# Optimization experiments

Hardware: AMD Instinct MI355X
Metric: run time of the kernel (lower is better)

The kernel has to match this reference:

```python
import jax, jax.numpy as jnp
import numpy as np

N_NODES = 100000

def gcn_conv(x, W, b, src, dst, n):
    # PyG GCNConv with add_self_loops=True, symmetric normalization.
    # Transform first (reduces feature dim before irregular aggregation).
    h = x @ W  # [N, out]
    # degree with self loops: in-degree over dst plus 1 per node
    deg = jax.ops.segment_sum(jnp.ones_like(dst, dtype=h.dtype), dst, num_segments=n) + 1.0
    dinv = jax.lax.rsqrt(deg)  # deg >= 1 due to self loops
    norm = dinv[src] * dinv[dst]  # [E]
    # message = norm * h[src], aggregated at dst; self-loop term = dinv_i^2 * h_i
    agg = jax.ops.segment_sum(h[src] * norm[:, None], dst, num_segments=n)
    agg = agg + h * (dinv * dinv)[:, None]
    return agg + b

def setup_inputs() -> dict:
    key = jax.random.key(0)
    k1, k2, k3, k4, k5 = jax.random.split(key, 5)
    F_in, H, E_dim = 128, 64, 64
    node_features = jax.random.normal(k1, (N_NODES, F_in), dtype=jnp.float32)
    edge_index = jax.random.randint(k2, (2, 1600000), 0, N_NODES, dtype=jnp.int64)
    s = 1.0 / np.sqrt(F_in)
    W1 = jax.random.uniform(k3, (F_in, H), jnp.float32, -s, s)
    b1 = jnp.zeros((H,), jnp.float32)
    s2 = 1.0 / np.sqrt(H)
    W2 = jax.random.uniform(k4, (H, H), jnp.float32, -s2, s2)
    b2 = jnp.zeros((H,), jnp.float32)
    Wl = jax.random.uniform(k5, (H, E_dim), jnp.float32, -s2, s2)
    bl = jnp.zeros((E_dim,), jnp.float32)
    return {"node_features": node_features, "edge_index": edge_index,
            "W1": W1, "b1": b1, "W2": W2, "b2": b2, "Wl": Wl, "bl": bl}

def reference(node_features, edge_index, W1, b1, W2, b2, Wl, bl):
    src, dst = edge_index[0], edge_index[1]
    n = node_features.shape[0]
    x = node_features.astype(jnp.float32)
    x = jax.nn.relu(gcn_conv(x, W1, b1, src, dst, n))
    # dropout: train=False -> identity
    x = jax.nn.relu(gcn_conv(x, W2, b2, src, dst, n))
    x = x @ Wl + bl
    return jax.nn.sigmoid(x).T  # [embed_size, N]
```

## Files before the change

kernel.cpp:

```cpp
#include <hip/hip_runtime.h>
#include <hip/hip_bf16.h>


#define FEAT 64
#define FIN 128
#define PAD 64
#define SUBC 4
#define SUBCAP 1280
#define CAP (SUBC * SUBCAP)
#define EPB 8192
#define MAXNB 512

typedef __attribute__((ext_vector_type(8))) short  short8;
typedef __attribute__((ext_vector_type(4))) float  f32x4;
typedef __attribute__((ext_vector_type(2))) float  float2v;

__device__ __forceinline__ unsigned short f2bf(float f) {
    union { float f; unsigned u; } x; x.f = f;
    unsigned r = x.u + 0x7FFF + ((x.u >> 16) & 1);
    return (unsigned short)(r >> 16);
}
__device__ __forceinline__ float bflo(unsigned u) {
    union { unsigned v; float f; } x; x.v = u << 16; return x.f;
}
__device__ __forceinline__ float bfhi(unsigned u) {
    union { unsigned v; float f; } x; x.v = u & 0xFFFF0000u; return x.f;
}

__global__ void wtrans_kernel(const float* __restrict__ W1, const float* __restrict__ W2,
                              const float* __restrict__ Wl,
                              unsigned short* __restrict__ Wt1, unsigned short* __restrict__ Wt2,
                              unsigned short* __restrict__ Wlt, int* __restrict__ bcnt) {
    int t = blockIdx.x * 256 + threadIdx.x;
    if (t < FIN * 64) {
        int k = t >> 6, n = t & 63;
        Wt1[n * FIN + k] = f2bf(W1[t]);
    } else if (t < FIN * 64 + 64 * 64) {
        int u = t - FIN * 64;
        int k = u >> 6, n = u & 63;
        Wt2[n * 64 + k] = f2bf(W2[u]);
    } else if (t < FIN * 64 + 2 * 64 * 64) {
        int u = t - FIN * 64 - 64 * 64;
        int k = u >> 6, n = u & 63;
        Wlt[n * 64 + k] = f2bf(Wl[u]);
    } else if (t < FIN * 64 + 2 * 64 * 64 + MAXNB * SUBC * 16) {
        bcnt[t - FIN * 64 - 2 * 64 * 64] = 0;
    }
}

__global__ __launch_bounds__(256) void bin_kernel(const int* __restrict__ ei,
                                                  int* __restrict__ bcnt,
                                                  int* __restrict__ bbuf,
                                                  int E, int nb) {
    __shared__ int hist[MAXNB];
    __shared__ int base[MAXNB];
    for (int t = threadIdx.x; t < nb; t += 256) hist[t] = 0;
    __syncthreads();
    int e0 = blockIdx.x * EPB;
    int sub = blockIdx.x & (SUBC - 1);
    int sreg[32], dreg[32], preg[32];
#pragma unroll
    for (int k = 0; k < 32; ++k) {
        int idx = e0 + k * 256 + threadIdx.x;
        if (idx < E) {
            sreg[k] = ei[idx];
            dreg[k] = ei[E + idx];
            preg[k] = atomicAdd(&hist[dreg[k] >> 8], 1);
        } else {
            dreg[k] = -1;
        }
    }
    __syncthreads();
    for (int t = threadIdx.x; t < nb; t += 256) {
        int h = hist[t];
        base[t] = (h > 0) ? atomicAdd(&bcnt[(t * SUBC + sub) * 16], h) : 0;
    }
    __syncthreads();
#pragma unroll
    for (int k = 0; k < 32; ++k) {
        if (dreg[k] >= 0) {
            int b = dreg[k] >> 8;
            int p = base[b] + preg[k];
            if (p < SUBCAP)
                bbuf[(size_t)b * CAP + sub * SUBCAP + p] = sreg[k] | ((dreg[k] & 255) << 20);
        }
    }
}

__global__ __launch_bounds__(256) void ell_from_bins_kernel(const int* __restrict__ bbuf,
                                                            const int* __restrict__ bcnt,
                                                            int* __restrict__ col,
                                                            int* __restrict__ cnt,
                                                            float* __restrict__ dinv,
                                                            unsigned int* __restrict__ gz,
                                                            int N) {
    __shared__ int lcnt[256];
    int b = blockIdx.x;
    int d0 = b << 8;
    lcnt[threadIdx.x] = 0;
    if (b == 0 && threadIdx.x < 32)
        gz[(size_t)N * 32 + threadIdx.x] = 0u;
    __syncthreads();
#pragma unroll
    for (int sub = 0; sub < SUBC; ++sub) {
        int ne = bcnt[(b * SUBC + sub) * 16];
        if (ne > SUBCAP) ne = SUBCAP;
        const int* eb = bbuf + (size_t)b * CAP + sub * SUBCAP;
        for (int i = threadIdx.x; i < ne; i += 256) {
            int w = eb[i];
            int s = w & 0xFFFFF;
            int dl = w >> 20;
            int slot = atomicAdd(&lcnt[dl], 1);
            if (slot < PAD) col[(size_t)(d0 + dl) * PAD + slot] = s;
        }
    }
    __syncthreads();
    int d = d0 + threadIdx.x;
    if (d < N) {
        int c = lcnt[threadIdx.x];
        if (c > PAD) c = PAD;
        int c8 = (c + 7) & ~7;
        for (int k = c; k < c8; ++k) col[(size_t)d * PAD + k] = N;
        cnt[d] = c;
        dinv[d] = rsqrtf((float)c + 1.0f);
    }
}

__global__ __launch_bounds__(256) void gemm1_mfma_kernel(const float* __restrict__ x,
                                                         const unsigned short* __restrict__ Wt,
                                                         const float* __restrict__ dinv,
                                                         unsigned short* __restrict__ g, int N) {
    const int lane = threadIdx.x & 63;
    const int wave = threadIdx.x >> 6;
    const int m = lane & 15, quad = lane >> 4;
    const int r0 = blockIdx.x * 64 + wave * 16;
    const int arow = r0 + m;
    const bool aok = arow < N;
    f32x4 acc[4] = {f32x4{0,0,0,0}, f32x4{0,0,0,0}, f32x4{0,0,0,0}, f32x4{0,0,0,0}};
    union { short8 s; unsigned short u[8]; } a;
#pragma unroll
    for (int s = 0; s < FIN / 32; ++s) {
        if (aok) {
            const float* xp = x + (size_t)arow * FIN + s * 32 + quad * 8;
            float4 a0 = *(const float4*)xp;
            float4 a1 = *(const float4*)(xp + 4);
            a.u[0] = f2bf(a0.x); a.u[1] = f2bf(a0.y);
            a.u[2] = f2bf(a0.z); a.u[3] = f2bf(a0.w);
            a.u[4] = f2bf(a1.x); a.u[5] = f2bf(a1.y);
            a.u[6] = f2bf(a1.z); a.u[7] = f2bf(a1.w);
        } else {
#pragma unroll
            for (int k = 0; k < 8; ++k) a.u[k] = 0;
        }
#pragma unroll
        for (int t = 0; t < 4; ++t) {
            const unsigned short* bp = Wt + (size_t)(t * 16 + m) * FIN + s * 32 + quad * 8;
            short8 bf = *(const short8*)bp;
            acc[t] = __builtin_amdgcn_mfma_f32_16x16x32_bf16(a.s, bf, acc[t], 0, 0, 0);
        }
    }
    const int rbase = r0 + quad * 4;
#pragma unroll
    for (int i = 0; i < 4; ++i) {
        int r = rbase + i;
        if (r < N) {
            float di = dinv[r];
#pragma unroll
            for (int t = 0; t < 4; ++t)
                g[(size_t)r * 64 + t * 16 + m] = f2bf(di * acc[t][i]);
        }
    }
}

__global__ __launch_bounds__(256) void gemm2_mfma_kernel(const unsigned short* __restrict__ xb,
                                                         const unsigned short* __restrict__ Wt,
                                                         const float* __restrict__ dinv,
                                                         unsigned short* __restrict__ g, int N) {
    const int lane = threadIdx.x & 63;
    const int wave = threadIdx.x >> 6;
    const int m = lane & 15, quad = lane >> 4;
    const int r0 = blockIdx.x * 64 + wave * 16;
    const int arow = r0 + m;
    const bool aok = arow < N;
    f32x4 acc[4] = {f32x4{0,0,0,0}, f32x4{0,0,0,0}, f32x4{0,0,0,0}, f32x4{0,0,0,0}};
    const short8 zero8 = short8{0,0,0,0,0,0,0,0};
#pragma unroll
    for (int s = 0; s < 2; ++s) {
        short8 a = aok ? *(const short8*)(xb + (size_t)arow * 64 + s * 32 + quad * 8) : zero8;
#pragma unroll
        for (int t = 0; t < 4; ++t) {
            short8 bf = *(const short8*)(Wt + (size_t)(t * 16 + m) * 64 + s * 32 + quad * 8);
            acc[t] = __builtin_amdgcn_mfma_f32_16x16x32_bf16(a, bf, acc[t], 0, 0, 0);
        }
    }
    const int rbase = r0 + quad * 4;
#pragma unroll
    for (int i = 0; i < 4; ++i) {
        int r = rbase + i;
        if (r < N) {
            float di = dinv[r];
#pragma unroll
            for (int t = 0; t < 4; ++t)
                g[(size_t)r * 64 + t * 16 + m] = f2bf(di * acc[t][i]);
        }
    }
}

__global__ __launch_bounds__(256) void agg_relu_kernel(const unsigned short* __restrict__ g,
                                                       const int* __restrict__ cnt,
                                                       const int* __restrict__ col,
                                                       const float* __restrict__ dinv,
                                                       const float* __restrict__ b,
                                                       unsigned short* __restrict__ xout, int N) {
    const int lane = threadIdx.x & 63;
    const int wave = threadIdx.x >> 6;
    const int ng = lane >> 3, fc = lane & 7;
    const int node = blockIdx.x * 32 + wave * 8 + ng;
    const bool valid = node < N;
    int c8 = 0;
    if (valid) {
        int c = cnt[node];
        if (c > PAD) c = PAD;
        c8 = (c + 7) & ~7;
    }
    int cmax = c8;
#pragma unroll
    for (int mk = 8; mk <= 32; mk <<= 1) {
        int o = __shfl_xor(cmax, mk, 64);
        cmax = cmax > o ? cmax : o;
    }
    const int* cl = col + (size_t)node * PAD;
    float2v acc0 = {0.f, 0.f}, acc1 = {0.f, 0.f}, acc2 = {0.f, 0.f}, acc3 = {0.f, 0.f};
    {
        uint4 w = *(const uint4*)(g + (size_t)(valid ? node : N) * 64 + fc * 8);
        acc0 += (float2v){bflo(w.x), bfhi(w.x)};
        acc1 += (float2v){bflo(w.y), bfhi(w.y)};
        acc2 += (float2v){bflo(w.z), bfhi(w.z)};
        acc3 += (float2v){bflo(w.w), bfhi(w.w)};
    }
    for (int j = 0; j < cmax; j += 4) {
        bool ok = j < c8;
        int s0 = ok ? cl[j]     : N;
        int s1 = ok ? cl[j + 1] : N;
        int s2 = ok ? cl[j + 2] : N;
        int s3 = ok ? cl[j + 3] : N;
        uint4 w0 = *(const uint4*)(g + (size_t)s0 * 64 + fc * 8);
        uint4 w1 = *(const uint4*)(g + (size_t)s1 * 64 + fc * 8);
        uint4 w2 = *(const uint4*)(g + (size_t)s2 * 64 + fc * 8);
        uint4 w3 = *(const uint4*)(g + (size_t)s3 * 64 + fc * 8);
        acc0 += (float2v){bflo(w0.x), bfhi(w0.x)};
        acc1 += (float2v){bflo(w0.y), bfhi(w0.y)};
        acc2 += (float2v){bflo(w0.z), bfhi(w0.z)};
        acc3 += (float2v){bflo(w0.w), bfhi(w0.w)};
        acc0 += (float2v){bflo(w1.x), bfhi(w1.x)};
        acc1 += (float2v){bflo(w1.y), bfhi(w1.y)};
        acc2 += (float2v){bflo(w1.z), bfhi(w1.z)};
        acc3 += (float2v){bflo(w1.w), bfhi(w1.w)};
        acc0 += (float2v){bflo(w2.x), bfhi(w2.x)};
        acc1 += (float2v){bflo(w2.y), bfhi(w2.y)};
        acc2 += (float2v){bflo(w2.z), bfhi(w2.z)};
        acc3 += (float2v){bflo(w2.w), bfhi(w2.w)};
        acc0 += (float2v){bflo(w3.x), bfhi(w3.x)};
        acc1 += (float2v){bflo(w3.y), bfhi(w3.y)};
        acc2 += (float2v){bflo(w3.z), bfhi(w3.z)};
        acc3 += (float2v){bflo(w3.w), bfhi(w3.w)};
    }
    if (valid) {
        float di = dinv[node];
        float4 b0 = *(const float4*)&b[fc * 8];
        float4 b1 = *(const float4*)&b[fc * 8 + 4];
        union { uint4 v; unsigned short u[8]; } o;
        o.u[0] = f2bf(fmaxf(di * acc0.x + b0.x, 0.f));
        o.u[1] = f2bf(fmaxf(di * acc0.y + b0.y, 0.f));
        o.u[2] = f2bf(fmaxf(di * acc1.x + b0.z, 0.f));
        o.u[3] = f2bf(fmaxf(di * acc1.y + b0.w, 0.f));
        o.u[4] = f2bf(fmaxf(di * acc2.x + b1.x, 0.f));
        o.u[5] = f2bf(fmaxf(di * acc2.y + b1.y, 0.f));
        o.u[6] = f2bf(fmaxf(di * acc3.x + b1.z, 0.f));
        o.u[7] = f2bf(fmaxf(di * acc3.y + b1.w, 0.f));
        *(uint4*)&xout[(size_t)node * 64 + fc * 8] = o.v;
    }
}

__global__ __launch_bounds__(256) void final_mfma_kernel(const unsigned short* __restrict__ x2,
                                                         const unsigned short* __restrict__ Wlt,
                                                         const float* __restrict__ bl,
                                                         float* __restrict__ out, int N) {
    const int lane = threadIdx.x & 63;
    const int wave = threadIdx.x >> 6;
    const int m = lane & 15, quad = lane >> 4;
    const int r0 = blockIdx.x * 64 + wave * 16;
    const int arow = r0 + m;
    const bool aok = arow < N;
    f32x4 acc[4] = {f32x4{0,0,0,0}, f32x4{0,0,0,0}, f32x4{0,0,0,0}, f32x4{0,0,0,0}};
    const short8 zero8 = short8{0,0,0,0,0,0,0,0};
#pragma unroll
    for (int s = 0; s < 2; ++s) {
        short8 a = aok ? *(const short8*)(x2 + (size_t)arow * 64 + s * 32 + quad * 8) : zero8;
#pragma unroll
        for (int t = 0; t < 4; ++t) {
            short8 bf = *(const short8*)(Wlt + (size_t)(t * 16 + m) * 64 + s * 32 + quad * 8);
            acc[t] = __builtin_amdgcn_mfma_f32_16x16x32_bf16(a, bf, acc[t], 0, 0, 0);
        }
    }
    const int rbase = r0 + quad * 4;
    if (rbase + 3 < N && (N & 3) == 0) {
#pragma unroll
        for (int t = 0; t < 4; ++t) {
            int j = t * 16 + m;
            float bj = bl[j];
            float4 o;
            o.x = 1.f / (1.f + __expf(-(acc[t][0] + bj)));
            o.y = 1.f / (1.f + __expf(-(acc[t][1] + bj)));
            o.z = 1.f / (1.f + __expf(-(acc[t][2] + bj)));
            o.w = 1.f / (1.f + __expf(-(acc[t][3] + bj)));
            *(float4*)&out[(size_t)j * N + rbase] = o;
        }
    } else {
#pragma unroll
        for (int t = 0; t < 4; ++t) {
            int j = t * 16 + m;
            float bj = bl[j];
#pragma unroll
            for (int i = 0; i < 4; ++i) {
                int r = rbase + i;
                if (r < N)
                    out[(size_t)j * N + r] = 1.f / (1.f + __expf(-(acc[t][i] + bj)));
            }
        }
    }
}

extern "C" void kernel_launch(void* const* d_in, const int* in_sizes, int n_in,
                              void* d_out, int out_size, void* d_ws, size_t ws_size,
                              hipStream_t stream) {
    const float* x   = (const float*)d_in[0];
    const int*   ei  = (const int*)d_in[1];
    const float* W1  = (const float*)d_in[2];
    const float* b1  = (const float*)d_in[3];
    const float* W2  = (const float*)d_in[4];
    const float* b2  = (const float*)d_in[5];
    const float* Wl  = (const float*)d_in[6];
    const float* bl  = (const float*)d_in[7];
    float*       out = (float*)d_out;

    int N  = in_sizes[0] / FIN;
    int E  = in_sizes[1] / 2;
    int nb = (N + 255) >> 8;
    int ng = (N + 63) >> 6;

    int*            bcnt = (int*)d_ws;
    unsigned short* Wt1  = (unsigned short*)(bcnt + MAXNB * SUBC * 16);
    unsigned short* Wt2  = Wt1 + FIN * 64;
    unsigned short* Wlt  = Wt2 + 64 * 64;
    int*            cnt  = (int*)(Wlt + 64 * 64);
    float*          dinv = (float*)(cnt + N);
    int*            col  = (int*)(dinv + N);
    int*            bbuf = col + (size_t)N * PAD;
    unsigned short* bufG = (unsigned short*)bbuf;
    unsigned short* bufX = bufG + (size_t)(N + 1) * FEAT;

    int wtot = FIN * 64 + 2 * 64 * 64 + MAXNB * SUBC * 16;
    wtrans_kernel<<<(wtot + 255) / 256, 256, 0, stream>>>(W1, W2, Wl, Wt1, Wt2, Wlt, bcnt);

    bin_kernel<<<(E + EPB - 1) / EPB, 256, 0, stream>>>(ei, bcnt, bbuf, E, nb);
    ell_from_bins_kernel<<<nb, 256, 0, stream>>>(bbuf, bcnt, col, cnt, dinv,
                                                 (unsigned int*)bufG, N);

    gemm1_mfma_kernel<<<ng, 256, 0, stream>>>(x, Wt1, dinv, bufG, N);
    agg_relu_kernel<<<(N + 31) / 32, 256, 0, stream>>>(bufG, cnt, col, dinv, b1, bufX, N);

    gemm2_mfma_kernel<<<ng, 256, 0, stream>>>(bufX, Wt2, dinv, bufG, N);
    agg_relu_kernel<<<(N + 31) / 32, 256, 0, stream>>>(bufG, cnt, col, dinv, b2, bufX, N);

    final_mfma_kernel<<<ng, 256, 0, stream>>>(bufX, Wlt, bl, out, N);
}
```

Measured before the change: 251.5 us.

## Fuse aggregation with following GEMMs via shared-memory tile

Merges each aggregation+ReLU pass with the next dense transform (W2 or the final linear+sigmoid) in one 512-thread block. The aggregated 64-node tile is staged in LDS and fed to MFMA, so the intermediate activations no longer round-trip through global memory and two launches go away. The dinv array is dropped and rsqrt is recomputed from cnt wherever it is needed. The gather loop now loads column indices with int4 vector loads and handles 8 neighbours per iteration. The block-wide barrier and extra LDS may reduce occupancy. The per-node ELL count is no longer clamped to PAD before use, which only matters if a node has more than PAD in-edges.

```diff
diff --git a/kernel.cpp b/kernel.cpp
--- a/kernel.cpp
+++ b/kernel.cpp
@@ -91,15 +91,17 @@
                                                             const int* __restrict__ bcnt,
                                                             int* __restrict__ col,
                                                             int* __restrict__ cnt,
-                                                            float* __restrict__ dinv,
                                                             unsigned int* __restrict__ gz,
+                                                            unsigned int* __restrict__ gz2,
                                                             int N) {
     __shared__ int lcnt[256];
     int b = blockIdx.x;
     int d0 = b << 8;
     lcnt[threadIdx.x] = 0;
-    if (b == 0 && threadIdx.x < 32)
+    if (b == 0 && threadIdx.x < 32) {
         gz[(size_t)N * 32 + threadIdx.x] = 0u;
+        gz2[(size_t)N * 32 + threadIdx.x] = 0u;
+    }
     __syncthreads();
 #pragma unroll
     for (int sub = 0; sub < SUBC; ++sub) {
@@ -122,13 +124,12 @@
         int c8 = (c + 7) & ~7;
         for (int k = c; k < c8; ++k) col[(size_t)d * PAD + k] = N;
         cnt[d] = c;
-        dinv[d] = rsqrtf((float)c + 1.0f);
     }
 }
 
 __global__ __launch_bounds__(256) void gemm1_mfma_kernel(const float* __restrict__ x,
                                                          const unsigned short* __restrict__ Wt,
-                                                         const float* __restrict__ dinv,
+                                                         const int* __restrict__ cnt,
                                                          unsigned short* __restrict__ g, int N) {
     const int lane = threadIdx.x & 63;
     const int wave = threadIdx.x >> 6;
@@ -164,7 +165,7 @@
     for (int i = 0; i < 4; ++i) {
         int r = rbase + i;
         if (r < N) {
-            float di = dinv[r];
+            float di = rsqrtf((float)cnt[r] + 1.0f);
 #pragma unroll
             for (int t = 0; t < 4; ++t)
                 g[(size_t)r * 64 + t * 16 + m] = f2bf(di * acc[t][i]);
@@ -172,142 +173,161 @@
     }
 }
 
-__global__ __launch_bounds__(256) void gemm2_mfma_kernel(const unsigned short* __restrict__ xb,
-                                                         const unsigned short* __restrict__ Wt,
-                                                         const float* __restrict__ dinv,
-                                                         unsigned short* __restrict__ g, int N) {
-    const int lane = threadIdx.x & 63;
-    const int wave = threadIdx.x >> 6;
+
+#define AGG_PHASE(bvec)                                                          \
+    const int lane = threadIdx.x & 63;                                           \
+    const int wave = threadIdx.x >> 6;                                           \
+    const int ngi = lane >> 3, fc = lane & 7;                                    \
+    const int nloc = wave * 8 + ngi;                                             \
+    const int node = blockIdx.x * 64 + nloc;                                     \
+    const bool valid = node < N;                                                 \
+    int c8 = 0;                                                                  \
+    float di = 0.f;                                                              \
+    if (valid) {                                                                 \
+        int c = cnt[node];                                                       \
+        di = rsqrtf((float)c + 1.0f);                                            \
+        c8 = (c + 7) & ~7;                                                       \
+    }                                                                            \
+    int cmax = c8;                                                               \
+    _Pragma("unroll")                                                            \
+    for (int mk = 8; mk <= 32; mk <<= 1) {                                       \
+        int o = __shfl_xor(cmax, mk, 64);                                        \
+        cmax = cmax > o ? cmax : o;                                              \
+    }                                                                            \
+    const int* cl = col + (size_t)node * PAD;                                    \
+    float2v acc0 = {0.f, 0.f}, acc1 = {0.f, 0.f}, acc2 = {0.f, 0.f}, acc3 = {0.f, 0.f}; \
+    {                                                                            \
+        uint4 w = *(const uint4*)(g + (size_t)(valid ? node : N) * 64 + fc * 8); \
+        acc0 += (float2v){bflo(w.x), bfhi(w.x)};                                 \
+        acc1 += (float2v){bflo(w.y), bfhi(w.y)};                                 \
+        acc2 += (float2v){bflo(w.z), bfhi(w.z)};                                 \
+        acc3 += (float2v){bflo(w.w), bfhi(w.w)};                                 \
+    }                                                                            \
+    const int4 sent = {N, N, N, N};                                              \
+    for (int j = 0; j < cmax; j += 8) {                                          \
+        bool ok = j < c8;                                                        \
+        int4 ca = ok ? *(const int4*)(cl + j)     : sent;                        \
+        int4 cb = ok ? *(const int4*)(cl + j + 4) : sent;                        \
+        uint4 w0 = *(const uint4*)(g + (size_t)ca.x * 64 + fc * 8);              \
+        uint4 w1 = *(const uint4*)(g + (size_t)ca.y * 64 + fc * 8);              \
+        uint4 w2 = *(const uint4*)(g + (size_t)ca.z * 64 + fc * 8);              \
+        uint4 w3 = *(const uint4*)(g + (size_t)ca.w * 64 + fc * 8);              \
+        uint4 w4 = *(const uint4*)(g + (size_t)cb.x * 64 + fc * 8);              \
+        uint4 w5 = *(const uint4*)(g + (size_t)cb.y * 64 + fc * 8);              \
+        uint4 w6 = *(const uint4*)(g + (size_t)cb.z * 64 + fc * 8);              \
+        uint4 w7 = *(const uint4*)(g + (size_t)cb.w * 64 + fc * 8);              \
+        acc0 += (float2v){bflo(w0.x), bfhi(w0.x)};                               \
+        acc1 += (float2v){bflo(w0.y), bfhi(w0.y)};                               \
+        acc2 += (float2v){bflo(w0.z), bfhi(w0.z)};                               \
+        acc3 += (float2v){bflo(w0.w), bfhi(w0.w)};                               \
+        acc0 += (float2v){bflo(w1.x), bfhi(w1.x)};                               \
+        acc1 += (float2v){bflo(w1.y), bfhi(w1.y)};                               \
+        acc2 += (float2v){bflo(w1.z), bfhi(w1.z)};                               \
+        acc3 += (float2v){bflo(w1.w), bfhi(w1.w)};                               \
+        acc0 += (float2v){bflo(w2.x), bfhi(w2.x)};                               \
+        acc1 += (float2v){bflo(w2.y), bfhi(w2.y)};                               \
+        acc2 += (float2v){bflo(w2.z), bfhi(w2.z)};                               \
+        acc3 += (float2v){bflo(w2.w), bfhi(w2.w)};                               \
+        acc0 += (float2v){bflo(w3.x), bfhi(w3.x)};                               \
+        acc1 += (float2v){bflo(w3.y), bfhi(w3.y)};                               \
+        acc2 += (float2v){bflo(w3.z), bfhi(w3.z)};                               \
+        acc3 += (float2v){bflo(w3.w), bfhi(w3.w)};                               \
+        acc0 += (float2v){bflo(w4.x), bfhi(w4.x)};                               \
+        acc1 += (float2v){bflo(w4.y), bfhi(w4.y)};                               \
+        acc2 += (float2v){bflo(w4.z), bfhi(w4.z)};                               \
+        acc3 += (float2v){bflo(w4.w), bfhi(w4.w)};                               \
+        acc0 += (float2v){bflo(w5.x), bfhi(w5.x)};                               \
+        acc1 += (float2v){bflo(w5.y), bfhi(w5.y)};                               \
+        acc2 += (float2v){bflo(w5.z), bfhi(w5.z)};                               \
+        acc3 += (float2v){bflo(w5.w), bfhi(w5.w)};                               \
+        acc0 += (float2v){bflo(w6.x), bfhi(w6.x)};                               \
+        acc1 += (float2v){bflo(w6.y), bfhi(w6.y)};                               \
+        acc2 += (float2v){bflo(w6.z), bfhi(w6.z)};                               \
+        acc3 += (float2v){bflo(w6.w), bfhi(w6.w)};                               \
+        acc0 += (float2v){bflo(w7.x), bfhi(w7.x)};                               \
+        acc1 += (float2v){bflo(w7.y), bfhi(w7.y)};                               \
+        acc2 += (float2v){bflo(w7.z), bfhi(w7.z)};                               \
+        acc3 += (float2v){bflo(w7.w), bfhi(w7.w)};                               \
+    }                                                                            \
+    {                                                                            \
+        float4 b0 = *(const float4*)&bvec[fc * 8];                               \
+        float4 b1 = *(const float4*)&bvec[fc * 8 + 4];                           \
+        union { uint4 v; unsigned short u[8]; } o;                               \
+        o.u[0] = f2bf(fmaxf(di * acc0.x + b0.x, 0.f));                           \
+        o.u[1] = f2bf(fmaxf(di * acc0.y + b0.y, 0.f));                           \
+        o.u[2] = f2bf(fmaxf(di * acc1.x + b0.z, 0.f));                           \
+        o.u[3] = f2bf(fmaxf(di * acc1.y + b0.w, 0.f));                           \
+        o.u[4] = f2bf(fmaxf(di * acc2.x + b1.x, 0.f));                           \
+        o.u[5] = f2bf(fmaxf(di * acc2.y + b1.y, 0.f));                           \
+        o.u[6] = f2bf(fmaxf(di * acc3.x + b1.z, 0.f));                           \
+        o.u[7] = f2bf(fmaxf(di * acc3.y + b1.w, 0.f));                           \
+        *(uint4*)&tile[nloc][fc * 8] = o.v;                                      \
+    }                                                                            \
+    __syncthreads();
+
+__global__ __launch_bounds__(512) void agg_gemm2_kernel(const unsigned short* __restrict__ g,
+                                                        const int* __restrict__ cnt,
+                                                        const int* __restrict__ col,
+                                                        const float* __restrict__ b,
+                                                        const unsigned short* __restrict__ Wt,
+                                                        unsigned short* __restrict__ gout,
+                                                        int N) {
+    __shared__ unsigned short tile[64][72];
+    AGG_PHASE(b)
+    const int v = wave & 3;
+    const int tb = (wave >> 2) * 2;
     const int m = lane & 15, quad = lane >> 4;
-    const int r0 = blockIdx.x * 64 + wave * 16;
-    const int arow = r0 + m;
-    const bool aok = arow < N;
-    f32x4 acc[4] = {f32x4{0,0,0,0}, f32x4{0,0,0,0}, f32x4{0,0,0,0}, f32x4{0,0,0,0}};
-    const short8 zero8 = short8{0,0,0,0,0,0,0,0};
+    f32x4 acc[2] = {f32x4{0,0,0,0}, f32x4{0,0,0,0}};
 #pragma unroll
     for (int s = 0; s < 2; ++s) {
-        short8 a = aok ? *(const short8*)(xb + (size_t)arow * 64 + s * 32 + quad * 8) : zero8;
-#pragma unroll
-        for (int t = 0; t < 4; ++t) {
-            short8 bf = *(const short8*)(Wt + (size_t)(t * 16 + m) * 64 + s * 32 + quad * 8);
+        short8 a = *(const short8*)&tile[v * 16 + m][s * 32 + quad * 8];
+#pragma unroll
+        for (int t = 0; t < 2; ++t) {
+            short8 bf = *(const short8*)(Wt + (size_t)((tb + t) * 16 + m) * 64 + s * 32 + quad * 8);
             acc[t] = __builtin_amdgcn_mfma_f32_16x16x32_bf16(a, bf, acc[t], 0, 0, 0);
         }
     }
-    const int rbase = r0 + quad * 4;
+    const int rbase = blockIdx.x * 64 + v * 16 + quad * 4;
 #pragma unroll
     for (int i = 0; i < 4; ++i) {
         int r = rbase + i;
         if (r < N) {
-            float di = dinv[r];
-#pragma unroll
-            for (int t = 0; t < 4; ++t)
-                g[(size_t)r * 64 + t * 16 + m] = f2bf(di * acc[t][i]);
-        }
-    }
-}
-
-__global__ __launch_bounds__(256) void agg_relu_kernel(const unsigned short* __restrict__ g,
-                                                       const int* __restrict__ cnt,
-                                                       const int* __restrict__ col,
-                                                       const float* __restrict__ dinv,
-                                                       const float* __restrict__ b,
-                                                       unsigned short* __restrict__ xout, int N) {
-    const int lane = threadIdx.x & 63;
-    const int wave = threadIdx.x >> 6;
-    const int ng = lane >> 3, fc = lane & 7;
-    const int node = blockIdx.x * 32 + wave * 8 + ng;
-    const bool valid = node < N;
-    int c8 = 0;
-    if (valid) {
-        int c = cnt[node];
-        if (c > PAD) c = PAD;
-        c8 = (c + 7) & ~7;
-    }
-    int cmax = c8;
-#pragma unroll
-    for (int mk = 8; mk <= 32; mk <<= 1) {
-        int o = __shfl_xor(cmax, mk, 64);
-        cmax = cmax > o ? cmax : o;
-    }
-    const int* cl = col + (size_t)node * PAD;
-    float2v acc0 = {0.f, 0.f}, acc1 = {0.f, 0.f}, acc2 = {0.f, 0.f}, acc3 = {0.f, 0.f};
-    {
-        uint4 w = *(const uint4*)(g + (size_t)(valid ? node : N) * 64 + fc * 8);
-        acc0 += (float2v){bflo(w.x), bfhi(w.x)};
-        acc1 += (float2v){bflo(w.y), bfhi(w.y)};
-        acc2 += (float2v){bflo(w.z), bfhi(w.z)};
-        acc3 += (float2v){bflo(w.w), bfhi(w.w)};
-    }
-    for (int j = 0; j < cmax; j += 4) {
-        bool ok = j < c8;
-        int s0 = ok ? cl[j]     : N;
-        int s1 = ok ? cl[j + 1] : N;
-        int s2 = ok ? cl[j + 2] : N;
-        int s3 = ok ? cl[j + 3] : N;
-        uint4 w0 = *(const uint4*)(g + (size_t)s0 * 64 + fc * 8);
-        uint4 w1 = *(const uint4*)(g + (size_t)s1 * 64 + fc * 8);
-        uint4 w2 = *(const uint4*)(g + (size_t)s2 * 64 + fc * 8);
-        uint4 w3 = *(const uint4*)(g + (size_t)s3 * 64 + fc * 8);
-        acc0 += (float2v){bflo(w0.x), bfhi(w0.x)};
-        acc1 += (float2v){bflo(w0.y), bfhi(w0.y)};
-        acc2 += (float2v){bflo(w0.z), bfhi(w0.z)};
-        acc3 += (float2v){bflo(w0.w), bfhi(w0.w)};
-        acc0 += (float2v){bflo(w1.x), bfhi(w1.x)};
-        acc1 += (float2v){bflo(w1.y), bfhi(w1.y)};
-        acc2 += (float2v){bflo(w1.z), bfhi(w1.z)};
-        acc3 += (float2v){bflo(w1.w), bfhi(w1.w)};
-        acc0 += (float2v){bflo(w2.x), bfhi(w2.x)};
-        acc1 += (float2v){bflo(w2.y), bfhi(w2.y)};
-        acc2 += (float2v){bflo(w2.z), bfhi(w2.z)};
-        acc3 += (float2v){bflo(w2.w), bfhi(w2.w)};
-        acc0 += (float2v){bflo(w3.x), bfhi(w3.x)};
-        acc1 += (float2v){bflo(w3.y), bfhi(w3.y)};
-        acc2 += (float2v){bflo(w3.z), bfhi(w3.z)};
-        acc3 += (float2v){bflo(w3.w), bfhi(w3.w)};
-    }
-    if (valid) {
-        float di = dinv[node];
-        float4 b0 = *(const float4*)&b[fc * 8];
-        float4 b1 = *(const float4*)&b[fc * 8 + 4];
-        union { uint4 v; unsigned short u[8]; } o;
-        o.u[0] = f2bf(fmaxf(di * acc0.x + b0.x, 0.f));
-        o.u[1] = f2bf(fmaxf(di * acc0.y + b0.y, 0.f));
-        o.u[2] = f2bf(fmaxf(di * acc1.x + b0.z, 0.f));
-        o.u[3] = f2bf(fmaxf(di * acc1.y + b0.w, 0.f));
-        o.u[4] = f2bf(fmaxf(di * acc2.x + b1.x, 0.f));
-        o.u[5] = f2bf(fmaxf(di * acc2.y + b1.y, 0.f));
-        o.u[6] = f2bf(fmaxf(di * acc3.x + b1.z, 0.f));
-        o.u[7] = f2bf(fmaxf(di * acc3.y + b1.w, 0.f));
-        *(uint4*)&xout[(size_t)node * 64 + fc * 8] = o.v;
-    }
-}
-
-__global__ __launch_bounds__(256) void final_mfma_kernel(const unsigned short* __restrict__ x2,
-                                                         const unsigned short* __restrict__ Wlt,
-                                                         const float* __restrict__ bl,
-                                                         float* __restrict__ out, int N) {
-    const int lane = threadIdx.x & 63;
-    const int wave = threadIdx.x >> 6;
+            float dr = rsqrtf((float)cnt[r] + 1.0f);
+#pragma unroll
+            for (int t = 0; t < 2; ++t)
+                gout[(size_t)r * 64 + (tb + t) * 16 + m] = f2bf(dr * acc[t][i]);
+        }
+    }
+}
+
+__global__ __launch_bounds__(512) void agg_final_kernel(const unsigned short* __restrict__ g,
+                                                        const int* __restrict__ cnt,
+                                                        const int* __restrict__ col,
+                                                        const float* __restrict__ b,
+                                                        const unsigned short* __restrict__ Wt,
+                                                        const float* __restrict__ bl,
+                                                        float* __restrict__ out,
+                                                        int N) {
+    __shared__ unsigned short tile[64][72];
+    AGG_PHASE(b)
+    const int v = wave & 3;
+    const int tb = (wave >> 2) * 2;
     const int m = lane & 15, quad = lane >> 4;
-    const int r0 = blockIdx.x * 64 + wave * 16;
-    const int arow = r0 + m;
-    const bool aok = arow < N;
-    f32x4 acc[4] = {f32x4{0,0,0,0}, f32x4{0,0,0,0}, f32x4{0,0,0,0}, f32x4{0,0,0,0}};
-    const short8 zero8 = short8{0,0,0,0,0,0,0,0};
+    f32x4 acc[2] = {f32x4{0,0,0,0}, f32x4{0,0,0,0}};
 #pragma unroll
     for (int s = 0; s < 2; ++s) {
-        short8 a = aok ? *(const short8*)(x2 + (size_t)arow * 64 + s * 32 + quad * 8) : zero8;
-#pragma unroll
-        for (int t = 0; t < 4; ++t) {
-            short8 bf = *(const short8*)(Wlt + (size_t)(t * 16 + m) * 64 + s * 32 + quad * 8);
+        short8 a = *(const short8*)&tile[v * 16 + m][s * 32 + quad * 8];
+#pragma unroll
+        for (int t = 0; t < 2; ++t) {
+            short8 bf = *(const short8*)(Wt + (size_t)((tb + t) * 16 + m) * 64 + s * 32 + quad * 8);
             acc[t] = __builtin_amdgcn_mfma_f32_16x16x32_bf16(a, bf, acc[t], 0, 0, 0);
         }
     }
-    const int rbase = r0 + quad * 4;
-    if (rbase + 3 < N && (N & 3) == 0) {
-#pragma unroll
-        for (int t = 0; t < 4; ++t) {
-            int j = t * 16 + m;
+    const int rbase = blockIdx.x * 64 + v * 16 + quad * 4;
+    if (rbase + 3 < N) {
+#pragma unroll
+        for (int t = 0; t < 2; ++t) {
+            int j = (tb + t) * 16 + m;
             float bj = bl[j];
             float4 o;
             o.x = 1.f / (1.f + __expf(-(acc[t][0] + bj)));
@@ -318,8 +338,8 @@
         }
     } else {
 #pragma unroll
-        for (int t = 0; t < 4; ++t) {
-            int j = t * 16 + m;
+        for (int t = 0; t < 2; ++t) {
+            int j = (tb + t) * 16 + m;
             float bj = bl[j];
 #pragma unroll
             for (int i = 0; i < 4; ++i) {
@@ -354,24 +374,22 @@
     unsigned short* Wt2  = Wt1 + FIN * 64;
     unsigned short* Wlt  = Wt2 + 64 * 64;
     int*            cnt  = (int*)(Wlt + 64 * 64);
-    float*          dinv = (float*)(cnt + N);
-    int*            col  = (int*)(dinv + N);
+    int*            col  = cnt + N;
     int*            bbuf = col + (size_t)N * PAD;
     unsigned short* bufG = (unsigned short*)bbuf;
-    unsigned short* bufX = bufG + (size_t)(N + 1) * FEAT;
+    unsigned short* bufG2 = bufG + (size_t)(N + 1) * FEAT;
 
     int wtot = FIN * 64 + 2 * 64 * 64 + MAXNB * SUBC * 16;
     wtrans_kernel<<<(wtot + 255) / 256, 256, 0, stream>>>(W1, W2, Wl, Wt1, Wt2, Wlt, bcnt);
 
     bin_kernel<<<(E + EPB - 1) / EPB, 256, 0, stream>>>(ei, bcnt, bbuf, E, nb);
-    ell_from_bins_kernel<<<nb, 256, 0, stream>>>(bbuf, bcnt, col, cnt, dinv,
-                                                 (unsigned int*)bufG, N);
-
-    gemm1_mfma_kernel<<<ng, 256, 0, stream>>>(x, Wt1, dinv, bufG, N);
-    agg_relu_kernel<<<(N + 31) / 32, 256, 0, stream>>>(bufG, cnt, col, dinv, b1, bufX, N);
-
-    gemm2_mfma_kernel<<<ng, 256, 0, stream>>>(bufX, Wt2, dinv, bufG, N);
-    agg_relu_kernel<<<(N + 31) / 32, 256, 0, stream>>>(bufG, cnt, col, dinv, b2, bufX, N);
-
-    final_mfma_kernel<<<ng, 256, 0, stream>>>(bufX, Wlt, bl, out, N);
-}
+    ell_from_bins_kernel<<<nb, 256, 0, stream>>>(bbuf, bcnt, col, cnt,
+                                                 (unsigned int*)bufG,
+                                                 (unsigned int*)bufG2, N);
+
+    gemm1_mfma_kernel<<<ng, 256, 0, stream>>>(x, Wt1, cnt, bufG, N);
+
+    agg_gemm2_kernel<<<ng, 512, 0, stream>>>(bufG, cnt, col, b1, Wt2, bufG2, N);
+
+    agg_final_kernel<<<ng, 512, 0, stream>>>(bufG2, cnt, col, b2, Wlt, bl, out, N);
+}
```

New measurement: 231.7 us. 7.8% less time.
